# Kernel tuning notes

Hardware: AMD Instinct MI355X
Metric: run time of the kernel (lower is better)

## Reference

```python
import jax, jax.numpy as jnp
import numpy as np

B, T, H, IN, OUT, HORIZON = 65536, 15, 128, 6, 3, 10
LN_EPS = 1e-5


def _w(k, shape, s=0.08):
    return jax.random.normal(k, shape, jnp.float32) * s


def setup_inputs() -> dict:
    key = jax.random.key(0)
    ks = jax.random.split(key, 16)
    return {
        "x": jax.random.normal(ks[0], (B, T, IN), jnp.float32),
        # encoder layer 0 (input 6 -> 128), PyTorch LSTM gate order i,f,g,o
        "W_ih0": _w(ks[1], (4 * H, IN)), "W_hh0": _w(ks[2], (4 * H, H)), "b0": jnp.zeros((4 * H,), jnp.float32),
        # encoder layer 1 (128 -> 128)
        "W_ih1": _w(ks[3], (4 * H, H)), "W_hh1": _w(ks[4], (4 * H, H)), "b1": jnp.zeros((4 * H,), jnp.float32),
        # decoder LSTM (128 -> 128)
        "W_ihd": _w(ks[5], (4 * H, H)), "W_hhd": _w(ks[6], (4 * H, H)), "bd": jnp.zeros((4 * H,), jnp.float32),
        # step embedding [pred_horizon+1, H]
        "emb": _w(ks[7], (HORIZON + 1, H), 0.5),
        # decoder_input_proj: Linear(3+128 -> 128)
        "Wp": _w(ks[8], (H, OUT + H)), "bp": jnp.zeros((H,), jnp.float32),
        # heads
        "Wm": _w(ks[9], (OUT, H)), "bm": jnp.zeros((OUT,), jnp.float32),
        "Ws": _w(ks[10], (OUT, H)), "bs": jnp.zeros((OUT,), jnp.float32),
        # dec_ln
        "ln_g": jnp.ones((H,), jnp.float32), "ln_b": jnp.zeros((H,), jnp.float32),
    }


def _lstm_cell(h, c, x_t, Wih, Whh, b):
    g = x_t @ Wih.T + h @ Whh.T + b  # [B, 4H]
    i, f, gg, o = jnp.split(g, 4, axis=-1)
    c = jax.nn.sigmoid(f) * c + jax.nn.sigmoid(i) * jnp.tanh(gg)
    h = jax.nn.sigmoid(o) * jnp.tanh(c)
    return h, c


def _run_lstm_layer(seq, Wih, Whh, b):
    # seq: [B, T, D] -> outputs [B, T, H], final (h, c)
    n = seq.shape[0]
    h0 = jnp.zeros((n, H), seq.dtype)
    c0 = jnp.zeros((n, H), seq.dtype)

    def step(carry, xt):
        h, c = carry
        h, c = _lstm_cell(h, c, xt, Wih, Whh, b)
        return (h, c), h

    (h, c), outs = jax.lax.scan(step, (h0, c0), jnp.swapaxes(seq, 0, 1))
    return jnp.swapaxes(outs, 0, 1), h, c


def _layernorm(x, g, b):
    mu = jnp.mean(x, axis=-1, keepdims=True)
    var = jnp.mean(jnp.square(x - mu), axis=-1, keepdims=True)
    return (x - mu) * jax.lax.rsqrt(var + LN_EPS) * g + b


def reference(x, W_ih0, W_hh0, b0, W_ih1, W_hh1, b1, W_ihd, W_hhd, bd, emb, Wp, bp, Wm, bm, Ws, bs, ln_g, ln_b):
    # --- encoder: 2-layer LSTM (eval mode, no dropout) ---
    out0, _, _ = _run_lstm_layer(x, W_ih0, W_hh0, b0)
    _, h_enc, c_enc = _run_lstm_layer(out0, W_ih1, W_hh1, b1)

    prev0 = x[:, -1, :OUT]  # [B, 3]
    n = x.shape[0]

    def dstep(carry, step):
        h, c, prev = carry
        se = jnp.broadcast_to(emb[step], (n, H))
        dec_in = jax.nn.relu(jnp.concatenate([prev, se], axis=-1) @ Wp.T + bp)
        h, c = _lstm_cell(h, c, dec_in, W_ihd, W_hhd, bd)
        feat = _layernorm(h, ln_g, ln_b)
        mu = feat @ Wm.T + bm
        ls = jnp.clip(feat @ Ws.T + bs, -6.0, 3.0)
        prev = jax.lax.stop_gradient(mu)  # mu.detach()
        return (h, c, prev), (mu, ls)

    _, (mus, lss) = jax.lax.scan(dstep, (h_enc, c_enc, prev0), jnp.arange(HORIZON))
    means = jnp.swapaxes(mus, 0, 1)     # [B, HORIZON, 3]
    log_stds = jnp.swapaxes(lss, 0, 1)  # [B, HORIZON, 3]
    return means, log_stds
```

## Files before the change

kernel.cpp:

```cpp
#include <hip/hip_runtime.h>
#include <stdint.h>

typedef __attribute__((ext_vector_type(8))) short short8;
typedef __attribute__((ext_vector_type(4))) float f32x4;

#define NT 15

#define SET0 0
#define SET1 81920
#define SET2 212992
#define SET3 344064
#define PK_TOTAL 346112
#define DBASE_OFF (PK_TOTAL*2)

__device__ __forceinline__ unsigned short f2bf(float f){
  unsigned int u = __builtin_bit_cast(unsigned int, f);
  u += 0x7fffu + ((u >> 16) & 1u);
  return (unsigned short)(u >> 16);
}
__device__ __forceinline__ float sigf(float x){
  return __builtin_amdgcn_rcpf(1.0f + __expf(-x));
}
__device__ __forceinline__ float tanhf_(float x){
  return 1.0f - 2.0f*__builtin_amdgcn_rcpf(1.0f + __expf(2.0f*x));
}
__device__ __forceinline__ int sidx(int row, int col){
  return row*128 + (col ^ ((row & 7) << 3));
}

__global__ void pack_w(const float* __restrict__ Wih0, const float* __restrict__ Whh0,
                       const float* __restrict__ Wih1, const float* __restrict__ Whh1,
                       const float* __restrict__ Wihd, const float* __restrict__ Whhd,
                       const float* __restrict__ Wm,  const float* __restrict__ Ws,
                       unsigned short* __restrict__ pk)
{
  int idx = blockIdx.x*256 + threadIdx.x;
  if (idx >= PK_TOTAL) return;
  float v = 0.f;
  if (idx >= SET3){
    int e = idx - SET3;
    int j = e & 7, lane = (e >> 3) & 63, kt = e >> 9;
    int n = lane & 15;
    int k = kt*32 + (lane >> 4)*8 + j;
    if (n < 3) v = Wm[n*128 + k];
    else if (n < 6) v = Ws[(n-3)*128 + k];
  } else {
    int set, e;
    if (idx < SET1){ set = 0; e = idx; }
    else if (idx < SET2){ set = 1; e = idx - SET1; }
    else { set = 2; e = idx - SET2; }
    int j = e & 7, lane = (e >> 3) & 63, rest = e >> 9;
    int nf = (set == 0) ? 5 : 8;
    int kt = rest % nf, pair = rest / nf;
    int g = pair & 3, jt = pair >> 2;
    int n = g*128 + jt*16 + (lane & 15);
    int kk = (lane >> 4)*8 + j;
    if (set == 0){
      if (kt < 4) v = Whh0[n*128 + kt*32 + kk];
      else if (kk < 6) v = Wih0[n*6 + kk];
    } else {
      const float* Wi = (set == 1) ? Wih1 : Wihd;
      const float* Wh = (set == 1) ? Whh1 : Whhd;
      v = (kt < 4) ? Wi[n*128 + kt*32 + kk] : Wh[n*128 + (kt-4)*32 + kk];
    }
  }
  pk[idx] = f2bf(v);
}

__global__ void prep_decbase(const float* __restrict__ emb, const float* __restrict__ Wp,
                             const float* __restrict__ bp, float* __restrict__ dbase)
{
  int idx = blockIdx.x*128 + threadIdx.x;
  if (idx >= 1280) return;
  int s = idx >> 7, j = idx & 127;
  float acc = bp[j];
  for (int k = 0; k < 128; ++k) acc += emb[s*128 + k] * Wp[j*131 + 3 + k];
  dbase[idx] = acc;
}

__global__ __launch_bounds__(512)
void traj_main(const float* __restrict__ x,
               const unsigned short* __restrict__ pk,
               const float* __restrict__ dbase,
               const float* __restrict__ b0g, const float* __restrict__ b1g,
               const float* __restrict__ bdg,
               const float* __restrict__ Wp,
               const float* __restrict__ bm, const float* __restrict__ bs,
               const float* __restrict__ lng, const float* __restrict__ lnb,
               float* __restrict__ out)
{
  __shared__ __align__(16) unsigned short hP[3][64*128];
  __shared__ __align__(16) union {
    unsigned short xs[NT*64*8];
    struct { float om[64][30]; float os[64][30]; } o;
  } u2;
  __shared__ __align__(16) struct {
    float sred[8][64][2];
    float mus[64][2];
    float prevb[64][4];
  } u;

  const int tid  = threadIdx.x;
  const int w    = tid >> 6;
  const int lane = tid & 63;
  const int lidx = lane & 15;
  const int lgrp = lane >> 4;
  const int col  = w*16 + lidx;
  const int row0 = blockIdx.x * 64;

  for (int i = tid; i < 64*128; i += 512){ hP[0][i] = 0; hP[1][i] = 0; }
  for (int i = tid; i < NT*64*8; i += 512){
    int k8 = i & 7, rt = i >> 3;
    int r = rt & 63, t = rt >> 6;
    u2.xs[i] = (k8 < 6) ? f2bf(x[(size_t)(row0 + r)*90 + t*6 + k8])
                        : (unsigned short)0;
  }

  float b0v[4], b1v[4];
  #pragma unroll
  for (int g = 0; g < 4; ++g){ b0v[g] = b0g[g*128 + col]; b1v[g] = b1g[g*128 + col]; }

  float c0[4][4], c1[4][4];
  #pragma unroll
  for (int m = 0; m < 4; ++m)
    #pragma unroll
    for (int r = 0; r < 4; ++r){ c0[m][r] = 0.f; c1[m][r] = 0.f; }

  __syncthreads();

  const unsigned short* pw0 = pk + SET0 + (w*4)*(5*512) + lane*8;
  const unsigned short* pw1 = pk + SET1 + (w*4)*(8*512) + lane*8;

  int i0 = 0, i1 = 1, ifr = 2;
  #pragma unroll 1
  for (int t = 0; t < NT; ++t){
    const unsigned short* bh0 = &hP[i0][0];
    const unsigned short* bh1 = &hP[i1][0];
    unsigned short*       bnw = &hP[ifr][0];

    short8 w0f[4][5];
    #pragma unroll
    for (int g = 0; g < 4; ++g)
      #pragma unroll
      for (int kt = 0; kt < 5; ++kt)
        w0f[g][kt] = *(const short8*)&pw0[(g*5 + kt)*512];
    #pragma unroll
    for (int m = 0; m < 4; ++m){
      const int arow = m*16 + lidx;
      short8 a[5];
      #pragma unroll
      for (int kt = 0; kt < 4; ++kt)
        a[kt] = *(const short8*)&bh0[sidx(arow, kt*32 + lgrp*8)];
      short8 ax = {0,0,0,0,0,0,0,0};
      if (lgrp == 0) ax = *(const short8*)&u2.xs[(t*64 + arow)*8];
      a[4] = ax;
      f32x4 acc[4];
      #pragma unroll
      for (int g = 0; g < 4; ++g){
        f32x4 s = {0.f,0.f,0.f,0.f};
        #pragma unroll
        for (int kt = 0; kt < 5; ++kt)
          s = __builtin_amdgcn_mfma_f32_16x16x32_bf16(a[kt], w0f[g][kt], s, 0, 0, 0);
        acc[g] = s;
      }
      #pragma unroll
      for (int r = 0; r < 4; ++r){
        float iv = sigf(acc[0][r] + b0v[0]);
        float fv = sigf(acc[1][r] + b0v[1]);
        float gv = tanhf_(acc[2][r] + b0v[2]);
        float ov = sigf(acc[3][r] + b0v[3]);
        float c = fv*c0[m][r] + iv*gv;
        c0[m][r] = c;
        bnw[sidx(m*16 + lgrp*4 + r, col)] = f2bf(ov*tanhf_(c));
      }
    }
    __syncthreads();

    short8 w1f[4][8];
    #pragma unroll
    for (int g = 0; g < 4; ++g)
      #pragma unroll
      for (int kt = 0; kt < 8; ++kt)
        w1f[g][kt] = *(const short8*)&pw1[(g*8 + kt)*512];
    #pragma unroll
    for (int m = 0; m < 4; ++m){
      const int arow = m*16 + lidx;
      short8 a[8];
      #pragma unroll
      for (int kt = 0; kt < 4; ++kt)
        a[kt] = *(const short8*)&bnw[sidx(arow, kt*32 + lgrp*8)];
      #pragma unroll
      for (int kt = 0; kt < 4; ++kt)
        a[4+kt] = *(const short8*)&bh1[sidx(arow, kt*32 + lgrp*8)];
      f32x4 acc[4];
      #pragma unroll
      for (int g = 0; g < 4; ++g){
        f32x4 s = {0.f,0.f,0.f,0.f};
        #pragma unroll
        for (int kt = 0; kt < 8; ++kt)
          s = __builtin_amdgcn_mfma_f32_16x16x32_bf16(a[kt], w1f[g][kt], s, 0, 0, 0);
        acc[g] = s;
      }
      #pragma unroll
      for (int r = 0; r < 4; ++r){
        float iv = sigf(acc[0][r] + b1v[0]);
        float fv = sigf(acc[1][r] + b1v[1]);
        float gv = tanhf_(acc[2][r] + b1v[2]);
        float ov = sigf(acc[3][r] + b1v[3]);
        float c = fv*c1[m][r] + iv*gv;
        c1[m][r] = c;
        const_cast<unsigned short*>(bh0)[sidx(m*16 + lgrp*4 + r, col)] =
            f2bf(ov*tanhf_(c));
      }
    }
    __syncthreads();
    int t0 = i0; i0 = ifr; ifr = i1; i1 = t0;
  }

  const unsigned short* pw2 = pk + SET2 + (w*4)*(8*512) + lane*8;
  short8 wdf[4][8];
  #pragma unroll
  for (int g = 0; g < 4; ++g)
    #pragma unroll
    for (int kt = 0; kt < 8; ++kt)
      wdf[g][kt] = *(const short8*)&pw2[(g*8 + kt)*512];
  short8 whf[4];
  {
    const short8 z8 = {0,0,0,0,0,0,0,0};
    #pragma unroll
    for (int kt = 0; kt < 4; ++kt) whf[kt] = z8;
    if (w < 4){
      #pragma unroll
      for (int kt = 0; kt < 4; ++kt)
        whf[kt] = *(const short8*)&pk[SET3 + kt*512 + lane*8];
    }
  }

  const float wpa = Wp[col*131 + 0], wpb = Wp[col*131 + 1], wpc = Wp[col*131 + 2];
  const float lngv = lng[col], lnbv = lnb[col];
  float bdv[4];
  #pragma unroll
  for (int g = 0; g < 4; ++g) bdv[g] = bdg[g*128 + col];
  float bmo = 0.f;
  if (lidx < 3) bmo = bm[lidx];
  else if (lidx < 6) bmo = bs[lidx - 3];

  __syncthreads();

  if (tid < 192){
    int r = tid / 3, o = tid - r*3;
    u.prevb[r][o] = x[(size_t)(row0 + r)*90 + 14*6 + o];
  }
  __syncthreads();

  int hcur = 1, hnew = 0;
  #pragma unroll 1
  for (int s = 0; s < 10; ++s){
    unsigned short* bdin = &hP[2][0];
    const unsigned short* bh = &hP[hcur][0];
    unsigned short* bhn = &hP[hnew][0];

    const float dbs = dbase[s*128 + col];
    #pragma unroll
    for (int m = 0; m < 4; ++m)
      #pragma unroll
      for (int r = 0; r < 4; ++r){
        const int row = m*16 + lgrp*4 + r;
        f32x4 pv = *(const f32x4*)&u.prevb[row][0];
        float v = dbs + pv[0]*wpa + pv[1]*wpb + pv[2]*wpc;
        bdin[sidx(row, col)] = f2bf(v > 0.f ? v : 0.f);
      }
    __syncthreads();

    float hv[4][4];
    #pragma unroll
    for (int m = 0; m < 4; ++m){
      const int arow = m*16 + lidx;
      short8 a[8];
      #pragma unroll
      for (int kt = 0; kt < 4; ++kt)
        a[kt] = *(const short8*)&bdin[sidx(arow, kt*32 + lgrp*8)];
      #pragma unroll
      for (int kt = 0; kt < 4; ++kt)
        a[4+kt] = *(const short8*)&bh[sidx(arow, kt*32 + lgrp*8)];
      f32x4 acc[4];
      #pragma unroll
      for (int g = 0; g < 4; ++g){
        f32x4 sa = {0.f,0.f,0.f,0.f};
        #pragma unroll
        for (int kt = 0; kt < 8; ++kt)
          sa = __builtin_amdgcn_mfma_f32_16x16x32_bf16(a[kt], wdf[g][kt], sa, 0, 0, 0);
        acc[g] = sa;
      }
      #pragma unroll
      for (int r = 0; r < 4; ++r){
        float iv = sigf(acc[0][r] + bdv[0]);
        float fv = sigf(acc[1][r] + bdv[1]);
        float gv = tanhf_(acc[2][r] + bdv[2]);
        float ov = sigf(acc[3][r] + bdv[3]);
        float c = fv*c1[m][r] + iv*gv;
        c1[m][r] = c;
        float h = ov*tanhf_(c);
        hv[m][r] = h;
        bhn[sidx(m*16 + lgrp*4 + r, col)] = f2bf(h);
      }
    }
    {
      float s1[4][4], s2[4][4];
      #pragma unroll
      for (int m = 0; m < 4; ++m)
        #pragma unroll
        for (int r = 0; r < 4; ++r){ s1[m][r] = hv[m][r]; s2[m][r] = hv[m][r]*hv[m][r]; }
      #pragma unroll
      for (int d = 1; d < 16; d <<= 1)
        #pragma unroll
        for (int m = 0; m < 4; ++m)
          #pragma unroll
          for (int r = 0; r < 4; ++r){
            s1[m][r] += __shfl_xor(s1[m][r], d);
            s2[m][r] += __shfl_xor(s2[m][r], d);
          }
      if (lidx == 0){
        #pragma unroll
        for (int m = 0; m < 4; ++m)
          #pragma unroll
          for (int r = 0; r < 4; ++r){
            u.sred[w][m*16 + lgrp*4 + r][0] = s1[m][r];
            u.sred[w][m*16 + lgrp*4 + r][1] = s2[m][r];
          }
      }
    }
    __syncthreads();
    if (tid < 64){
      float ss = 0.f, sq = 0.f;
      #pragma unroll
      for (int ww = 0; ww < 8; ++ww){ ss += u.sred[ww][tid][0]; sq += u.sred[ww][tid][1]; }
      float mu = ss * (1.f/128.f);
      float var = sq * (1.f/128.f) - mu*mu;
      u.mus[tid][0] = mu;
      u.mus[tid][1] = __builtin_amdgcn_rsqf(var + 1e-5f);
    }
    __syncthreads();
    #pragma unroll
    for (int m = 0; m < 4; ++m)
      #pragma unroll
      for (int r = 0; r < 4; ++r){
        const int row = m*16 + lgrp*4 + r;
        float mu = u.mus[row][0], rs = u.mus[row][1];
        bdin[sidx(row, col)] = f2bf((hv[m][r] - mu)*rs*lngv + lnbv);
      }
    __syncthreads();
    if (w < 4){
      const int arow = w*16 + lidx;
      short8 a[4];
      #pragma unroll
      for (int kt = 0; kt < 4; ++kt)
        a[kt] = *(const short8*)&bdin[sidx(arow, kt*32 + lgrp*8)];
      f32x4 acc = {0.f,0.f,0.f,0.f};
      #pragma unroll
      for (int kt = 0; kt < 4; ++kt)
        acc = __builtin_amdgcn_mfma_f32_16x16x32_bf16(a[kt], whf[kt], acc, 0, 0, 0);
      #pragma unroll
      for (int r = 0; r < 4; ++r){
        const int row = w*16 + lgrp*4 + r;
        float v = acc[r] + bmo;
        if (lidx < 3){
          u2.o.om[row][s*3 + lidx] = v;
          u.prevb[row][lidx] = v;
        } else if (lidx < 6){
          u2.o.os[row][s*3 + (lidx - 3)] = fminf(fmaxf(v, -6.f), 3.f);
        }
      }
    }
    __syncthreads();
    int tswap = hcur; hcur = hnew; hnew = tswap;
  }

  for (int i = tid; i < 1920; i += 512){
    int r = i / 30, cx = i - r*30;
    out[(size_t)(row0 + r)*30 + cx] = u2.o.om[r][cx];
    out[(size_t)65536*30 + (size_t)(row0 + r)*30 + cx] = u2.o.os[r][cx];
  }
}

extern "C" void kernel_launch(void* const* d_in, const int* in_sizes, int n_in,
                              void* d_out, int out_size, void* d_ws, size_t ws_size,
                              hipStream_t stream)
{
  const float* x    = (const float*)d_in[0];
  const float* Wih0 = (const float*)d_in[1];
  const float* Whh0 = (const float*)d_in[2];
  const float* b0   = (const float*)d_in[3];
  const float* Wih1 = (const float*)d_in[4];
  const float* Whh1 = (const float*)d_in[5];
  const float* b1   = (const float*)d_in[6];
  const float* Wihd = (const float*)d_in[7];
  const float* Whhd = (const float*)d_in[8];
  const float* bd   = (const float*)d_in[9];
  const float* emb  = (const float*)d_in[10];
  const float* Wp   = (const float*)d_in[11];
  const float* bp   = (const float*)d_in[12];
  const float* Wm   = (const float*)d_in[13];
  const float* bm   = (const float*)d_in[14];
  const float* Ws   = (const float*)d_in[15];
  const float* bs   = (const float*)d_in[16];
  const float* lng  = (const float*)d_in[17];
  const float* lnb  = (const float*)d_in[18];

  unsigned short* pkw = (unsigned short*)d_ws;
  float* dbase = (float*)((char*)d_ws + DBASE_OFF);

  pack_w<<<(PK_TOTAL + 255)/256, 256, 0, stream>>>(Wih0, Whh0, Wih1, Whh1,
                                                   Wihd, Whhd, Wm, Ws, pkw);
  prep_decbase<<<10, 128, 0, stream>>>(emb, Wp, bp, dbase);
  traj_main<<<1024, 512, 0, stream>>>(x, pkw, dbase, b0, b1, bd, Wp,
                                      bm, bs, lng, lnb, (float*)d_out);
}
```

Measured before the change: 2.296 ms.

## Fold LayerNorm into heads, restructure MFMA loops, stream weights per k-tile

The LayerNorm+head projection is rewritten algebraically: gamma is folded into the head weights and beta into the biases, so each row only needs sums of h, h^2 and h·w' reduced across the block. This removes the normalized-activation LDS round trip, an extra MFMA pass and two barriers per decoder step. The LSTM GEMMs are reordered to loop over k-tiles outermost, with bias-initialized accumulators for all four row tiles and weights loaded per k-tile from global instead of held in registers. __syncthreads is replaced by an explicit lgkmcnt wait plus s_barrier. The risks are more accumulator registers, more global weight reloads, and a slight change in numerics from computing variance through the folded form.

```diff
diff --git a/kernel.cpp b/kernel.cpp
--- a/kernel.cpp
+++ b/kernel.cpp
@@ -11,7 +11,7 @@
 #define SET2 212992
 #define SET3 344064
 #define PK_TOTAL 346112
-#define DBASE_OFF (PK_TOTAL*2)
+#define DD_OFF (PK_TOTAL*2)
 
 __device__ __forceinline__ unsigned short f2bf(float f){
   unsigned int u = __builtin_bit_cast(unsigned int, f);
@@ -26,6 +26,10 @@
 }
 __device__ __forceinline__ int sidx(int row, int col){
   return row*128 + (col ^ ((row & 7) << 3));
+}
+__device__ __forceinline__ void BAR(){
+  asm volatile("s_waitcnt lgkmcnt(0)" ::: "memory");
+  __builtin_amdgcn_s_barrier();
 }
 
 __global__ void pack_w(const float* __restrict__ Wih0, const float* __restrict__ Whh0,
@@ -67,26 +71,45 @@
   pk[idx] = f2bf(v);
 }
 
-__global__ void prep_decbase(const float* __restrict__ emb, const float* __restrict__ Wp,
-                             const float* __restrict__ bp, float* __restrict__ dbase)
+__global__ void prep_dec(const float* __restrict__ emb, const float* __restrict__ Wp,
+                         const float* __restrict__ bp,
+                         const float* __restrict__ Wm, const float* __restrict__ Ws,
+                         const float* __restrict__ bm, const float* __restrict__ bs,
+                         const float* __restrict__ lng, const float* __restrict__ lnb,
+                         float* __restrict__ dd)
 {
   int idx = blockIdx.x*128 + threadIdx.x;
-  if (idx >= 1280) return;
-  int s = idx >> 7, j = idx & 127;
-  float acc = bp[j];
-  for (int k = 0; k < 128; ++k) acc += emb[s*128 + k] * Wp[j*131 + 3 + k];
-  dbase[idx] = acc;
+  if (idx < 1280){
+    int s = idx >> 7, j = idx & 127;
+    float acc = bp[j];
+    for (int k = 0; k < 128; ++k) acc += emb[s*128 + k] * Wp[j*131 + 3 + k];
+    dd[idx] = acc;
+  } else if (idx < 2048){
+    int e = idx - 1280; int o = e >> 7, j = e & 127;
+    const float* W = (o < 3) ? (Wm + o*128) : (Ws + (o-3)*128);
+    dd[idx] = W[j] * lng[j];
+  } else if (idx < 2054){
+    int o = idx - 2048;
+    const float* W = (o < 3) ? (Wm + o*128) : (Ws + (o-3)*128);
+    float a = 0.f;
+    for (int k = 0; k < 128; ++k) a += W[k]*lng[k];
+    dd[idx] = a;
+  } else if (idx < 2060){
+    int o = idx - 2054;
+    const float* W = (o < 3) ? (Wm + o*128) : (Ws + (o-3)*128);
+    float a = (o < 3) ? bm[o] : bs[o-3];
+    for (int k = 0; k < 128; ++k) a += W[k]*lnb[k];
+    dd[idx] = a;
+  }
 }
 
 __global__ __launch_bounds__(512)
 void traj_main(const float* __restrict__ x,
                const unsigned short* __restrict__ pk,
-               const float* __restrict__ dbase,
+               const float* __restrict__ dd,
                const float* __restrict__ b0g, const float* __restrict__ b1g,
                const float* __restrict__ bdg,
                const float* __restrict__ Wp,
-               const float* __restrict__ bm, const float* __restrict__ bs,
-               const float* __restrict__ lng, const float* __restrict__ lnb,
                float* __restrict__ out)
 {
   __shared__ __align__(16) unsigned short hP[3][64*128];
@@ -95,8 +118,7 @@
     struct { float om[64][30]; float os[64][30]; } o;
   } u2;
   __shared__ __align__(16) struct {
-    float sred[8][64][2];
-    float mus[64][2];
+    float sred[8][64][8];
     float prevb[64][4];
   } u;
 
@@ -130,6 +152,8 @@
 
   const unsigned short* pw0 = pk + SET0 + (w*4)*(5*512) + lane*8;
   const unsigned short* pw1 = pk + SET1 + (w*4)*(8*512) + lane*8;
+  const unsigned short* pw2 = pk + SET2 + (w*4)*(8*512) + lane*8;
+  const short8 z8 = {0,0,0,0,0,0,0,0};
 
   int i0 = 0, i1 = 1, ifr = 2;
   #pragma unroll 1
@@ -138,114 +162,105 @@
     const unsigned short* bh1 = &hP[i1][0];
     unsigned short*       bnw = &hP[ifr][0];
 
-    short8 w0f[4][5];
-    #pragma unroll
-    for (int g = 0; g < 4; ++g)
-      #pragma unroll
-      for (int kt = 0; kt < 5; ++kt)
-        w0f[g][kt] = *(const short8*)&pw0[(g*5 + kt)*512];
-    #pragma unroll
-    for (int m = 0; m < 4; ++m){
-      const int arow = m*16 + lidx;
-      short8 a[5];
-      #pragma unroll
-      for (int kt = 0; kt < 4; ++kt)
-        a[kt] = *(const short8*)&bh0[sidx(arow, kt*32 + lgrp*8)];
-      short8 ax = {0,0,0,0,0,0,0,0};
-      if (lgrp == 0) ax = *(const short8*)&u2.xs[(t*64 + arow)*8];
-      a[4] = ax;
-      f32x4 acc[4];
-      #pragma unroll
-      for (int g = 0; g < 4; ++g){
-        f32x4 s = {0.f,0.f,0.f,0.f};
-        #pragma unroll
-        for (int kt = 0; kt < 5; ++kt)
-          s = __builtin_amdgcn_mfma_f32_16x16x32_bf16(a[kt], w0f[g][kt], s, 0, 0, 0);
-        acc[g] = s;
-      }
-      #pragma unroll
-      for (int r = 0; r < 4; ++r){
-        float iv = sigf(acc[0][r] + b0v[0]);
-        float fv = sigf(acc[1][r] + b0v[1]);
-        float gv = tanhf_(acc[2][r] + b0v[2]);
-        float ov = sigf(acc[3][r] + b0v[3]);
-        float c = fv*c0[m][r] + iv*gv;
-        c0[m][r] = c;
-        bnw[sidx(m*16 + lgrp*4 + r, col)] = f2bf(ov*tanhf_(c));
-      }
+    {
+      f32x4 acc[4][4];
+      #pragma unroll
+      for (int m = 0; m < 4; ++m)
+        #pragma unroll
+        for (int g = 0; g < 4; ++g)
+          acc[m][g] = (f32x4){b0v[g], b0v[g], b0v[g], b0v[g]};
+      #pragma unroll
+      for (int kt = 0; kt < 5; ++kt){
+        short8 am[4];
+        #pragma unroll
+        for (int m = 0; m < 4; ++m){
+          if (kt < 4)
+            am[m] = *(const short8*)&bh0[sidx(m*16 + lidx, kt*32 + lgrp*8)];
+          else
+            am[m] = (lgrp == 0) ? *(const short8*)&u2.xs[(t*64 + m*16 + lidx)*8] : z8;
+        }
+        #pragma unroll
+        for (int g = 0; g < 4; ++g){
+          short8 wv = *(const short8*)&pw0[(g*5 + kt)*512];
+          #pragma unroll
+          for (int m = 0; m < 4; ++m)
+            acc[m][g] = __builtin_amdgcn_mfma_f32_16x16x32_bf16(am[m], wv, acc[m][g], 0, 0, 0);
+        }
+      }
+      #pragma unroll
+      for (int m = 0; m < 4; ++m)
+        #pragma unroll
+        for (int r = 0; r < 4; ++r){
+          float iv = sigf(acc[m][0][r]);
+          float fv = sigf(acc[m][1][r]);
+          float gv = tanhf_(acc[m][2][r]);
+          float ov = sigf(acc[m][3][r]);
+          float c = fv*c0[m][r] + iv*gv;
+          c0[m][r] = c;
+          bnw[sidx(m*16 + lgrp*4 + r, col)] = f2bf(ov*tanhf_(c));
+        }
     }
-    __syncthreads();
-
-    short8 w1f[4][8];
-    #pragma unroll
-    for (int g = 0; g < 4; ++g)
-      #pragma unroll
-      for (int kt = 0; kt < 8; ++kt)
-        w1f[g][kt] = *(const short8*)&pw1[(g*8 + kt)*512];
-    #pragma unroll
-    for (int m = 0; m < 4; ++m){
-      const int arow = m*16 + lidx;
-      short8 a[8];
-      #pragma unroll
-      for (int kt = 0; kt < 4; ++kt)
-        a[kt] = *(const short8*)&bnw[sidx(arow, kt*32 + lgrp*8)];
-      #pragma unroll
-      for (int kt = 0; kt < 4; ++kt)
-        a[4+kt] = *(const short8*)&bh1[sidx(arow, kt*32 + lgrp*8)];
-      f32x4 acc[4];
-      #pragma unroll
-      for (int g = 0; g < 4; ++g){
-        f32x4 s = {0.f,0.f,0.f,0.f};
-        #pragma unroll
-        for (int kt = 0; kt < 8; ++kt)
-          s = __builtin_amdgcn_mfma_f32_16x16x32_bf16(a[kt], w1f[g][kt], s, 0, 0, 0);
-        acc[g] = s;
-      }
-      #pragma unroll
-      for (int r = 0; r < 4; ++r){
-        float iv = sigf(acc[0][r] + b1v[0]);
-        float fv = sigf(acc[1][r] + b1v[1]);
-        float gv = tanhf_(acc[2][r] + b1v[2]);
-        float ov = sigf(acc[3][r] + b1v[3]);
-        float c = fv*c1[m][r] + iv*gv;
-        c1[m][r] = c;
-        const_cast<unsigned short*>(bh0)[sidx(m*16 + lgrp*4 + r, col)] =
-            f2bf(ov*tanhf_(c));
-      }
+    BAR();
+
+    {
+      f32x4 acc[4][4];
+      #pragma unroll
+      for (int m = 0; m < 4; ++m)
+        #pragma unroll
+        for (int g = 0; g < 4; ++g)
+          acc[m][g] = (f32x4){b1v[g], b1v[g], b1v[g], b1v[g]};
+      #pragma unroll
+      for (int kt = 0; kt < 8; ++kt){
+        short8 am[4];
+        #pragma unroll
+        for (int m = 0; m < 4; ++m){
+          if (kt < 4)
+            am[m] = *(const short8*)&bnw[sidx(m*16 + lidx, kt*32 + lgrp*8)];
+          else
+            am[m] = *(const short8*)&bh1[sidx(m*16 + lidx, (kt-4)*32 + lgrp*8)];
+        }
+        #pragma unroll
+        for (int g = 0; g < 4; ++g){
+          short8 wv = *(const short8*)&pw1[(g*8 + kt)*512];
+          #pragma unroll
+          for (int m = 0; m < 4; ++m)
+            acc[m][g] = __builtin_amdgcn_mfma_f32_16x16x32_bf16(am[m], wv, acc[m][g], 0, 0, 0);
+        }
+      }
+      unsigned short* bwr = const_cast<unsigned short*>(bh0);
+      #pragma unroll
+      for (int m = 0; m < 4; ++m)
+        #pragma unroll
+        for (int r = 0; r < 4; ++r){
+          float iv = sigf(acc[m][0][r]);
+          float fv = sigf(acc[m][1][r]);
+          float gv = tanhf_(acc[m][2][r]);
+          float ov = sigf(acc[m][3][r]);
+          float c = fv*c1[m][r] + iv*gv;
+          c1[m][r] = c;
+          bwr[sidx(m*16 + lgrp*4 + r, col)] = f2bf(ov*tanhf_(c));
+        }
     }
-    __syncthreads();
+    BAR();
     int t0 = i0; i0 = ifr; ifr = i1; i1 = t0;
   }
 
-  const unsigned short* pw2 = pk + SET2 + (w*4)*(8*512) + lane*8;
-  short8 wdf[4][8];
-  #pragma unroll
-  for (int g = 0; g < 4; ++g)
-    #pragma unroll
-    for (int kt = 0; kt < 8; ++kt)
-      wdf[g][kt] = *(const short8*)&pw2[(g*8 + kt)*512];
-  short8 whf[4];
-  {
-    const short8 z8 = {0,0,0,0,0,0,0,0};
-    #pragma unroll
-    for (int kt = 0; kt < 4; ++kt) whf[kt] = z8;
-    if (w < 4){
-      #pragma unroll
-      for (int kt = 0; kt < 4; ++kt)
-        whf[kt] = *(const short8*)&pk[SET3 + kt*512 + lane*8];
-    }
-  }
+  const float* dbase = dd;
+  const float* hwp   = dd + 1280;
+  const float* hbp   = dd + 2048;
+  const float* hcp   = dd + 2054;
 
   const float wpa = Wp[col*131 + 0], wpb = Wp[col*131 + 1], wpc = Wp[col*131 + 2];
-  const float lngv = lng[col], lnbv = lnb[col];
   float bdv[4];
   #pragma unroll
   for (int g = 0; g < 4; ++g) bdv[g] = bdg[g*128 + col];
-  float bmo = 0.f;
-  if (lidx < 3) bmo = bm[lidx];
-  else if (lidx < 6) bmo = bs[lidx - 3];
-
-  __syncthreads();
+  float hwv[6], hbv[6], hcv[6];
+  #pragma unroll
+  for (int o = 0; o < 6; ++o){
+    hwv[o] = hwp[o*128 + col];
+    hbv[o] = hbp[o];
+    hcv[o] = hcp[o];
+  }
 
   if (tid < 192){
     int r = tid / 3, o = tid - r*3;
@@ -270,109 +285,90 @@
         float v = dbs + pv[0]*wpa + pv[1]*wpb + pv[2]*wpc;
         bdin[sidx(row, col)] = f2bf(v > 0.f ? v : 0.f);
       }
-    __syncthreads();
-
-    float hv[4][4];
-    #pragma unroll
-    for (int m = 0; m < 4; ++m){
-      const int arow = m*16 + lidx;
-      short8 a[8];
-      #pragma unroll
-      for (int kt = 0; kt < 4; ++kt)
-        a[kt] = *(const short8*)&bdin[sidx(arow, kt*32 + lgrp*8)];
-      #pragma unroll
-      for (int kt = 0; kt < 4; ++kt)
-        a[4+kt] = *(const short8*)&bh[sidx(arow, kt*32 + lgrp*8)];
-      f32x4 acc[4];
-      #pragma unroll
-      for (int g = 0; g < 4; ++g){
-        f32x4 sa = {0.f,0.f,0.f,0.f};
-        #pragma unroll
-        for (int kt = 0; kt < 8; ++kt)
-          sa = __builtin_amdgcn_mfma_f32_16x16x32_bf16(a[kt], wdf[g][kt], sa, 0, 0, 0);
-        acc[g] = sa;
-      }
-      #pragma unroll
-      for (int r = 0; r < 4; ++r){
-        float iv = sigf(acc[0][r] + bdv[0]);
-        float fv = sigf(acc[1][r] + bdv[1]);
-        float gv = tanhf_(acc[2][r] + bdv[2]);
-        float ov = sigf(acc[3][r] + bdv[3]);
-        float c = fv*c1[m][r] + iv*gv;
-        c1[m][r] = c;
-        float h = ov*tanhf_(c);
-        hv[m][r] = h;
-        bhn[sidx(m*16 + lgrp*4 + r, col)] = f2bf(h);
-      }
+    BAR();
+
+    {
+      f32x4 acc[4][4];
+      #pragma unroll
+      for (int m = 0; m < 4; ++m)
+        #pragma unroll
+        for (int g = 0; g < 4; ++g)
+          acc[m][g] = (f32x4){bdv[g], bdv[g], bdv[g], bdv[g]};
+      #pragma unroll
+      for (int kt = 0; kt < 8; ++kt){
+        short8 am[4];
+        #pragma unroll
+        for (int m = 0; m < 4; ++m){
+          if (kt < 4)
+            am[m] = *(const short8*)&bdin[sidx(m*16 + lidx, kt*32 + lgrp*8)];
+          else
+            am[m] = *(const short8*)&bh[sidx(m*16 + lidx, (kt-4)*32 + lgrp*8)];
+        }
+        #pragma unroll
+        for (int g = 0; g < 4; ++g){
+          short8 wv = *(const short8*)&pw2[(g*8 + kt)*512];
+          #pragma unroll
+          for (int m = 0; m < 4; ++m)
+            acc[m][g] = __builtin_amdgcn_mfma_f32_16x16x32_bf16(am[m], wv, acc[m][g], 0, 0, 0);
+        }
+      }
+      #pragma unroll
+      for (int m = 0; m < 4; ++m)
+        #pragma unroll
+        for (int r = 0; r < 4; ++r){
+          float iv = sigf(acc[m][0][r]);
+          float fv = sigf(acc[m][1][r]);
+          float gv = tanhf_(acc[m][2][r]);
+          float ov = sigf(acc[m][3][r]);
+          float c = fv*c1[m][r] + iv*gv;
+          c1[m][r] = c;
+          float h = ov*tanhf_(c);
+          const int row = m*16 + lgrp*4 + r;
+          bhn[sidx(row, col)] = f2bf(h);
+          float vals[8];
+          vals[0] = h; vals[1] = h*h;
+          #pragma unroll
+          for (int o = 0; o < 6; ++o) vals[2+o] = h*hwv[o];
+          #pragma unroll
+          for (int d = 1; d < 16; d <<= 1)
+            #pragma unroll
+            for (int k = 0; k < 8; ++k)
+              vals[k] += __shfl_xor(vals[k], d);
+          if (lidx == 0){
+            *(f32x4*)&u.sred[w][row][0] = (f32x4){vals[0], vals[1], vals[2], vals[3]};
+            *(f32x4*)&u.sred[w][row][4] = (f32x4){vals[4], vals[5], vals[6], vals[7]};
+          }
+        }
     }
-    {
-      float s1[4][4], s2[4][4];
-      #pragma unroll
-      for (int m = 0; m < 4; ++m)
-        #pragma unroll
-        for (int r = 0; r < 4; ++r){ s1[m][r] = hv[m][r]; s2[m][r] = hv[m][r]*hv[m][r]; }
-      #pragma unroll
-      for (int d = 1; d < 16; d <<= 1)
-        #pragma unroll
-        for (int m = 0; m < 4; ++m)
-          #pragma unroll
-          for (int r = 0; r < 4; ++r){
-            s1[m][r] += __shfl_xor(s1[m][r], d);
-            s2[m][r] += __shfl_xor(s2[m][r], d);
-          }
-      if (lidx == 0){
-        #pragma unroll
-        for (int m = 0; m < 4; ++m)
-          #pragma unroll
-          for (int r = 0; r < 4; ++r){
-            u.sred[w][m*16 + lgrp*4 + r][0] = s1[m][r];
-            u.sred[w][m*16 + lgrp*4 + r][1] = s2[m][r];
-          }
+    BAR();
+
+    if (tid < 64){
+      float s1 = 0.f, s2 = 0.f;
+      float A[6] = {0.f, 0.f, 0.f, 0.f, 0.f, 0.f};
+      #pragma unroll
+      for (int ww = 0; ww < 8; ++ww){
+        f32x4 v0 = *(const f32x4*)&u.sred[ww][tid][0];
+        f32x4 v1 = *(const f32x4*)&u.sred[ww][tid][4];
+        s1 += v0[0]; s2 += v0[1];
+        A[0] += v0[2]; A[1] += v0[3];
+        A[2] += v1[0]; A[3] += v1[1]; A[4] += v1[2]; A[5] += v1[3];
+      }
+      float mu = s1 * (1.f/128.f);
+      float var = s2 * (1.f/128.f) - mu*mu;
+      float rs = __builtin_amdgcn_rsqf(var + 1e-5f);
+      #pragma unroll
+      for (int o = 0; o < 3; ++o){
+        float v = rs*(A[o] - mu*hbv[o]) + hcv[o];
+        u2.o.om[tid][s*3 + o] = v;
+        u.prevb[tid][o] = v;
+      }
+      #pragma unroll
+      for (int o = 3; o < 6; ++o){
+        float v = rs*(A[o] - mu*hbv[o]) + hcv[o];
+        u2.o.os[tid][s*3 + (o-3)] = fminf(fmaxf(v, -6.f), 3.f);
       }
     }
-    __syncthreads();
-    if (tid < 64){
-      float ss = 0.f, sq = 0.f;
-      #pragma unroll
-      for (int ww = 0; ww < 8; ++ww){ ss += u.sred[ww][tid][0]; sq += u.sred[ww][tid][1]; }
-      float mu = ss * (1.f/128.f);
-      float var = sq * (1.f/128.f) - mu*mu;
-      u.mus[tid][0] = mu;
-      u.mus[tid][1] = __builtin_amdgcn_rsqf(var + 1e-5f);
-    }
-    __syncthreads();
-    #pragma unroll
-    for (int m = 0; m < 4; ++m)
-      #pragma unroll
-      for (int r = 0; r < 4; ++r){
-        const int row = m*16 + lgrp*4 + r;
-        float mu = u.mus[row][0], rs = u.mus[row][1];
-        bdin[sidx(row, col)] = f2bf((hv[m][r] - mu)*rs*lngv + lnbv);
-      }
-    __syncthreads();
-    if (w < 4){
-      const int arow = w*16 + lidx;
-      short8 a[4];
-      #pragma unroll
-      for (int kt = 0; kt < 4; ++kt)
-        a[kt] = *(const short8*)&bdin[sidx(arow, kt*32 + lgrp*8)];
-      f32x4 acc = {0.f,0.f,0.f,0.f};
-      #pragma unroll
-      for (int kt = 0; kt < 4; ++kt)
-        acc = __builtin_amdgcn_mfma_f32_16x16x32_bf16(a[kt], whf[kt], acc, 0, 0, 0);
-      #pragma unroll
-      for (int r = 0; r < 4; ++r){
-        const int row = w*16 + lgrp*4 + r;
-        float v = acc[r] + bmo;
-        if (lidx < 3){
-          u2.o.om[row][s*3 + lidx] = v;
-          u.prevb[row][lidx] = v;
-        } else if (lidx < 6){
-          u2.o.os[row][s*3 + (lidx - 3)] = fminf(fmaxf(v, -6.f), 3.f);
-        }
-      }
-    }
-    __syncthreads();
+    BAR();
     int tswap = hcur; hcur = hnew; hnew = tswap;
   }
 
@@ -408,11 +404,10 @@
   const float* lnb  = (const float*)d_in[18];
 
   unsigned short* pkw = (unsigned short*)d_ws;
-  float* dbase = (float*)((char*)d_ws + DBASE_OFF);
+  float* dd = (float*)((char*)d_ws + DD_OFF);
 
   pack_w<<<(PK_TOTAL + 255)/256, 256, 0, stream>>>(Wih0, Whh0, Wih1, Whh1,
                                                    Wihd, Whhd, Wm, Ws, pkw);
-  prep_decbase<<<10, 128, 0, stream>>>(emb, Wp, bp, dbase);
-  traj_main<<<1024, 512, 0, stream>>>(x, pkw, dbase, b0, b1, bd, Wp,
-                                      bm, bs, lng, lnb, (float*)d_out);
-}
+  prep_dec<<<17, 128, 0, stream>>>(emb, Wp, bp, Wm, Ws, bm, bs, lng, lnb, dd);
+  traj_main<<<1024, 512, 0, stream>>>(x, pkw, dd, b0, b1, bd, Wp, (float*)d_out);
+}
```

Result: faster. 2.077 ms (-9.5%).
